# Kernel tuning notes

Measured on AMD Instinct MI355X. Metric: run time of the kernel, lower is better.

## Reference

```python
import jax, jax.numpy as jnp
import numpy as np

NB, S, D, B, T, KMAX = 7, 16, 128, 32, 2048, 31
KS = [31, 21, 15, 11, 7, 5, 3]  # per-band conv kernel sizes


def _ln(x, g, b, eps=1e-5):
    m = x.mean(-1, keepdims=True)
    v = ((x - m) ** 2).mean(-1, keepdims=True)
    return (x - m) * jax.lax.rsqrt(v + eps) * g + b


def setup_inputs() -> dict:
    key = jax.random.key(0)
    ks = jax.random.split(key, 18)
    n = lambda k, shape, s=0.02: jax.random.normal(k, shape, jnp.float32) * s
    # conv kernels zero-padded to KMAX=31; symmetric padding keeps SAME-conv
    # equivalent to Conv1d(kernel=k, padding=k//2)
    mask = np.zeros((NB, KMAX, 1, 1), np.float32)
    for i, k in enumerate(KS):
        off = (KMAX - k) // 2
        mask[i, off:off + k] = 1.0
    inp = {
        'x': jax.random.normal(ks[0], (B, T, S), jnp.float32),
        'conv_w': n(ks[1], (NB, KMAX, S, D)) * jnp.asarray(mask),
        'conv_b': n(ks[2], (NB, D)),
        'dec_g': jnp.ones((NB, D), jnp.float32),
        'dec_b': jnp.zeros((NB, D), jnp.float32),
        'n2_g': jnp.ones((NB, D), jnp.float32),
        'n2_b': jnp.zeros((NB, D), jnp.float32),
        'ffn_w1': n(ks[3], (NB, D, 2 * D)),
        'ffn_b1': n(ks[4], (NB, 2 * D)),
        'ffn_w2': n(ks[5], (NB, 2 * D, D)),
        'ffn_b2': n(ks[6], (NB, D)),
        'proj_w': n(ks[7], (NB, D, 4 * S)),
        'proj_b': n(ks[8], (NB, 4 * S)),
        'mix_w1': n(ks[9], (NB * 4 * S, 8 * S)),
        'mix_b1': n(ks[10], (8 * S,)),
        'mix_w2': n(ks[11], (8 * S, S)),
        'mix_b2': n(ks[12], (S,)),
    }
    return inp


def reference(x, conv_w, conv_b, dec_g, dec_b, n2_g, n2_b,
              ffn_w1, ffn_b1, ffn_w2, ffn_b2,
              proj_w, proj_b, mix_w1, mix_b1, mix_w2, mix_b2):
    # Spectral decomposition: per-band 1D conv + LayerNorm. [nb, B, T, D]
    conv1 = lambda w: jax.lax.conv_general_dilated(
        x, w, (1,), 'SAME', dimension_numbers=('NWC', 'WIO', 'NWC'))
    h = jax.vmap(conv1)(conv_w) + conv_b[:, None, None, :]
    h = _ln(h, dec_g[:, None, None, :], dec_b[:, None, None, :])
    # Band processors (empty history => residual FFN branch)
    z = _ln(h, n2_g[:, None, None, :], n2_b[:, None, None, :])
    u = jax.nn.gelu(jnp.einsum('nbtd,nde->nbte', z, ffn_w1)
                    + ffn_b1[:, None, None, :], approximate=False)
    band_out = h + (jnp.einsum('nbte,ned->nbtd', u, ffn_w2)
                    + ffn_b2[:, None, None, :])
    # Reconstruction: per-band projection, concat, mix MLP
    p = jnp.einsum('nbtd,ndp->nbtp', band_out, proj_w) + proj_b[:, None, None, :]
    cat = jnp.transpose(p, (1, 2, 0, 3)).reshape(x.shape[0], x.shape[1], -1)
    m = jax.nn.gelu(cat @ mix_w1 + mix_b1, approximate=False)
    return m @ mix_w2 + mix_b2
```

## Files before the change

kernel.cpp:

```cpp
#include <hip/hip_runtime.h>
#include <stdint.h>

#define NB   7
#define SIN  16
#define DD   128
#define BB   32
#define TT   2048
#define TM   64
#define KMAX 31

#define XWS  40
#define HS   136
#define US   264
#define PS   72

#define O_CWT 0
#define O_W1T 458752
#define O_W2T 688128
#define O_PT  917504
#define O_M1T 974848
#define O_M2T 1032192
#define W_TOTAL 1034240

typedef short v8s __attribute__((ext_vector_type(8)));
typedef float v4f __attribute__((ext_vector_type(4)));

__device__ __forceinline__ unsigned short f2b(float f) {
    unsigned u = __float_as_uint(f);
    u += 0x7fffu + ((u >> 16) & 1u);
    return (unsigned short)(u >> 16);
}
__device__ __forceinline__ float b2f(unsigned short h) {
    return __uint_as_float(((unsigned)h) << 16);
}
__device__ __forceinline__ float gelu_fast(float x) {
    return x / (1.f + __expf(-1.702f * x));
}
__device__ __forceinline__ float gelu_exact(float x) {
    return 0.5f * x * (1.f + erff(x * 0.70710678118654752f));
}

__global__ void prep_weights(const float* __restrict__ conv_w,
                             const float* __restrict__ ffn_w1,
                             const float* __restrict__ ffn_w2,
                             const float* __restrict__ proj_w,
                             const float* __restrict__ mix_w1,
                             const float* __restrict__ mix_w2,
                             unsigned short* __restrict__ wsb) {
    for (int i = blockIdx.x * 256 + threadIdx.x; i < W_TOTAL; i += gridDim.x * 256) {
        float v;
        int o = i;
        if (o < O_W1T) {
            int n = o / (128 * 512); int r = o % (128 * 512);
            int d = r / 512; int kf = r % 512;
            int k = kf >> 4, s = kf & 15;
            v = (k < KMAX) ? conv_w[((n * KMAX + k) * SIN + s) * DD + d] : 0.f;
        } else if ((o -= O_W1T) < (O_W2T - O_W1T)) {
            int n = o / (256 * 128); int r = o % (256 * 128);
            int e = r / 128; int k = r % 128;
            v = ffn_w1[(n * 128 + k) * 256 + e];
        } else if ((o -= (O_W2T - O_W1T)) < (O_PT - O_W2T)) {
            int n = o / (128 * 256); int r = o % (128 * 256);
            int d = r / 256; int e = r % 256;
            v = ffn_w2[(n * 256 + e) * 128 + d];
        } else if ((o -= (O_PT - O_W2T)) < (O_M1T - O_PT)) {
            int n = o / (64 * 128); int r = o % (64 * 128);
            int j = r / 128; int k = r % 128;
            v = proj_w[(n * 128 + k) * 64 + j];
        } else if ((o -= (O_M1T - O_PT)) < (O_M2T - O_M1T)) {
            int c = o / 448; int kk = o % 448;
            v = mix_w1[kk * 128 + c];
        } else {
            o -= (O_M2T - O_M1T);
            int o16 = o / 128; int c = o % 128;
            v = mix_w2[c * 16 + o16];
        }
        wsb[i] = f2b(v);
    }
}

__global__ __launch_bounds__(256, 2)
void fused_main(const float* __restrict__ x,
                const float* __restrict__ conv_b,
                const float* __restrict__ dec_g, const float* __restrict__ dec_b,
                const float* __restrict__ n2_g,  const float* __restrict__ n2_b,
                const float* __restrict__ ffn_b1, const float* __restrict__ ffn_b2,
                const float* __restrict__ proj_b,
                const float* __restrict__ mix_b1, const float* __restrict__ mix_b2,
                const unsigned short* __restrict__ wsb,
                float* __restrict__ out) {
    __shared__ __align__(16) unsigned short xw[95 * XWS];
    __shared__ __align__(16) unsigned short hbuf[TM * HS];
    __shared__ __align__(16) unsigned short zbuf[TM * HS];
    __shared__ __align__(16) unsigned short ubuf[TM * US];

    const int tid  = threadIdx.x;
    const int lane = tid & 63;
    const int w    = tid >> 6;
    const int l16  = lane & 15;
    const int quad = lane >> 4;
    const int bb   = blockIdx.x >> 5;
    const int t0   = (blockIdx.x & 31) * TM;

    const unsigned short* cwT = wsb + O_CWT;
    const unsigned short* w1T = wsb + O_W1T;
    const unsigned short* w2T = wsb + O_W2T;
    const unsigned short* pT  = wsb + O_PT;
    const unsigned short* m1T = wsb + O_M1T;
    const unsigned short* m2T = wsb + O_M2T;

    for (int i = tid; i < 95 * SIN; i += 256) {
        int r = i >> 4, s = i & 15;
        int t = t0 + r - 15;
        float v = (t >= 0 && t < TT) ? x[((long)bb * TT + t) * SIN + s] : 0.f;
        xw[r * XWS + s] = f2b(v);
    }

    v4f macc[4][2];
    #pragma unroll
    for (int a = 0; a < 4; a++)
        #pragma unroll
        for (int c = 0; c < 2; c++)
            macc[a][c] = (v4f){0.f, 0.f, 0.f, 0.f};

    __syncthreads();

    static const int lo_tab[NB] = {0, 64, 128, 160, 192, 192, 224};
    static const int hi_tab[NB] = {512, 416, 384, 352, 320, 288, 288};

    for (int n = 0; n < NB; ++n) {
        {
            v4f acc[4][2];
            #pragma unroll
            for (int mt = 0; mt < 4; mt++)
                #pragma unroll
                for (int nt = 0; nt < 2; nt++) acc[mt][nt] = (v4f){0.f, 0.f, 0.f, 0.f};
            const int colb = w * 32;
            const int lo = lo_tab[n], hi = hi_tab[n];
            for (int kf = lo; kf < hi; kf += 32) {
                const int tap  = (kf >> 4) + (quad >> 1);
                const int scol = (quad & 1) * 8;
                v8s a[4], bf[2];
                #pragma unroll
                for (int mt = 0; mt < 4; mt++)
                    a[mt] = *reinterpret_cast<const v8s*>(&xw[(mt * 16 + l16 + tap) * XWS + scol]);
                #pragma unroll
                for (int nt = 0; nt < 2; nt++)
                    bf[nt] = *reinterpret_cast<const v8s*>(
                        &cwT[(size_t)(n * 128 + colb + nt * 16 + l16) * 512 + kf + quad * 8]);
                #pragma unroll
                for (int mt = 0; mt < 4; mt++)
                    #pragma unroll
                    for (int nt = 0; nt < 2; nt++)
                        acc[mt][nt] = __builtin_amdgcn_mfma_f32_16x16x32_bf16(a[mt], bf[nt], acc[mt][nt], 0, 0, 0);
            }
            #pragma unroll
            for (int nt = 0; nt < 2; nt++) {
                const int col = colb + nt * 16 + l16;
                const float bias = conv_b[n * 128 + col];
                #pragma unroll
                for (int mt = 0; mt < 4; mt++)
                    #pragma unroll
                    for (int r = 0; r < 4; r++)
                        hbuf[(mt * 16 + quad * 4 + r) * HS + col] = f2b(acc[mt][nt][r] + bias);
            }
        }
        __syncthreads();

        {
            const int row = tid >> 2, q = tid & 3;
            float v[32], s1 = 0.f, s2 = 0.f;
            #pragma unroll
            for (int c8 = 0; c8 < 4; c8++) {
                v8s t8 = *reinterpret_cast<const v8s*>(&hbuf[row * HS + q * 32 + c8 * 8]);
                #pragma unroll
                for (int j = 0; j < 8; j++) {
                    float f = b2f((unsigned short)t8[j]);
                    v[c8 * 8 + j] = f; s1 += f; s2 += f * f;
                }
            }
            s1 += __shfl_xor(s1, 1); s2 += __shfl_xor(s2, 1);
            s1 += __shfl_xor(s1, 2); s2 += __shfl_xor(s2, 2);
            const float m1 = s1 * (1.f / 128.f);
            const float rs = rsqrtf(s2 * (1.f / 128.f) - m1 * m1 + 1e-5f);
            const float4* dg4 = (const float4*)(dec_g + n * 128);
            const float4* db4 = (const float4*)(dec_b + n * 128);
            float hv[32], t1 = 0.f, t2 = 0.f;
            #pragma unroll
            for (int c4 = 0; c4 < 8; c4++) {
                float4 g4 = dg4[q * 8 + c4], b4 = db4[q * 8 + c4];
                float ga[4] = {g4.x, g4.y, g4.z, g4.w};
                float ba[4] = {b4.x, b4.y, b4.z, b4.w};
                #pragma unroll
                for (int j = 0; j < 4; j++) {
                    float h = (v[c4 * 4 + j] - m1) * rs * ga[j] + ba[j];
                    hv[c4 * 4 + j] = h; t1 += h; t2 += h * h;
                    hbuf[row * HS + q * 32 + c4 * 4 + j] = f2b(h);
                }
            }
            t1 += __shfl_xor(t1, 1); t2 += __shfl_xor(t2, 1);
            t1 += __shfl_xor(t1, 2); t2 += __shfl_xor(t2, 2);
            const float m2 = t1 * (1.f / 128.f);
            const float rs2 = rsqrtf(t2 * (1.f / 128.f) - m2 * m2 + 1e-5f);
            const float4* ng4 = (const float4*)(n2_g + n * 128);
            const float4* nb4 = (const float4*)(n2_b + n * 128);
            #pragma unroll
            for (int c4 = 0; c4 < 8; c4++) {
                float4 g4 = ng4[q * 8 + c4], b4 = nb4[q * 8 + c4];
                float ga[4] = {g4.x, g4.y, g4.z, g4.w};
                float ba[4] = {b4.x, b4.y, b4.z, b4.w};
                #pragma unroll
                for (int j = 0; j < 4; j++) {
                    float z = (hv[c4 * 4 + j] - m2) * rs2 * ga[j] + ba[j];
                    zbuf[row * HS + q * 32 + c4 * 4 + j] = f2b(z);
                }
            }
        }
        __syncthreads();

        {
            v4f acc[4][4];
            #pragma unroll
            for (int mt = 0; mt < 4; mt++)
                #pragma unroll
                for (int et = 0; et < 4; et++) acc[mt][et] = (v4f){0.f, 0.f, 0.f, 0.f};
            const int eb = w * 64;
            #pragma unroll
            for (int kb = 0; kb < 128; kb += 32) {
                v8s a[4], bf[4];
                #pragma unroll
                for (int mt = 0; mt < 4; mt++)
                    a[mt] = *reinterpret_cast<const v8s*>(&zbuf[(mt * 16 + l16) * HS + kb + quad * 8]);
                #pragma unroll
                for (int et = 0; et < 4; et++)
                    bf[et] = *reinterpret_cast<const v8s*>(
                        &w1T[(size_t)(n * 256 + eb + et * 16 + l16) * 128 + kb + quad * 8]);
                #pragma unroll
                for (int mt = 0; mt < 4; mt++)
                    #pragma unroll
                    for (int et = 0; et < 4; et++)
                        acc[mt][et] = __builtin_amdgcn_mfma_f32_16x16x32_bf16(a[mt], bf[et], acc[mt][et], 0, 0, 0);
            }
            #pragma unroll
            for (int et = 0; et < 4; et++) {
                const int e = eb + et * 16 + l16;
                const float bias = ffn_b1[n * 256 + e];
                #pragma unroll
                for (int mt = 0; mt < 4; mt++)
                    #pragma unroll
                    for (int r = 0; r < 4; r++)
                        ubuf[(mt * 16 + quad * 4 + r) * US + e] = f2b(gelu_fast(acc[mt][et][r] + bias));
            }
        }
        __syncthreads();

        {
            v4f acc[4][2];
            #pragma unroll
            for (int mt = 0; mt < 4; mt++)
                #pragma unroll
                for (int nt = 0; nt < 2; nt++) acc[mt][nt] = (v4f){0.f, 0.f, 0.f, 0.f};
            const int dbs = w * 32;
            #pragma unroll
            for (int kb = 0; kb < 256; kb += 32) {
                v8s a[4], bf[2];
                #pragma unroll
                for (int mt = 0; mt < 4; mt++)
                    a[mt] = *reinterpret_cast<const v8s*>(&ubuf[(mt * 16 + l16) * US + kb + quad * 8]);
                #pragma unroll
                for (int nt = 0; nt < 2; nt++)
                    bf[nt] = *reinterpret_cast<const v8s*>(
                        &w2T[(size_t)(n * 128 + dbs + nt * 16 + l16) * 256 + kb + quad * 8]);
                #pragma unroll
                for (int mt = 0; mt < 4; mt++)
                    #pragma unroll
                    for (int nt = 0; nt < 2; nt++)
                        acc[mt][nt] = __builtin_amdgcn_mfma_f32_16x16x32_bf16(a[mt], bf[nt], acc[mt][nt], 0, 0, 0);
            }
            #pragma unroll
            for (int nt = 0; nt < 2; nt++) {
                const int col = dbs + nt * 16 + l16;
                const float bias = ffn_b2[n * 128 + col];
                #pragma unroll
                for (int mt = 0; mt < 4; mt++)
                    #pragma unroll
                    for (int r = 0; r < 4; r++) {
                        const int row = mt * 16 + quad * 4 + r;
                        float bo = acc[mt][nt][r] + bias + b2f(hbuf[row * HS + col]);
                        zbuf[row * HS + col] = f2b(bo);
                    }
            }
        }
        __syncthreads();

        {
            v4f acc[4];
            #pragma unroll
            for (int mt = 0; mt < 4; mt++) acc[mt] = (v4f){0.f, 0.f, 0.f, 0.f};
            const int j = w * 16 + l16;
            #pragma unroll
            for (int kb = 0; kb < 128; kb += 32) {
                v8s bf = *reinterpret_cast<const v8s*>(&pT[(size_t)(n * 64 + j) * 128 + kb + quad * 8]);
                #pragma unroll
                for (int mt = 0; mt < 4; mt++) {
                    v8s a = *reinterpret_cast<const v8s*>(&zbuf[(mt * 16 + l16) * HS + kb + quad * 8]);
                    acc[mt] = __builtin_amdgcn_mfma_f32_16x16x32_bf16(a, bf, acc[mt], 0, 0, 0);
                }
            }
            const float bias = proj_b[n * 64 + j];
            unsigned short* pb = ubuf;
            #pragma unroll
            for (int mt = 0; mt < 4; mt++)
                #pragma unroll
                for (int r = 0; r < 4; r++)
                    pb[(mt * 16 + quad * 4 + r) * PS + j] = f2b(acc[mt][r] + bias);
        }
        __syncthreads();

        {
            const unsigned short* pb = ubuf;
            #pragma unroll
            for (int kb = 0; kb < 64; kb += 32) {
                v8s a[4], bf[2];
                #pragma unroll
                for (int mt = 0; mt < 4; mt++)
                    a[mt] = *reinterpret_cast<const v8s*>(&pb[(mt * 16 + l16) * PS + kb + quad * 8]);
                #pragma unroll
                for (int nt = 0; nt < 2; nt++)
                    bf[nt] = *reinterpret_cast<const v8s*>(
                        &m1T[(size_t)(w * 32 + nt * 16 + l16) * 448 + n * 64 + kb + quad * 8]);
                #pragma unroll
                for (int mt = 0; mt < 4; mt++)
                    #pragma unroll
                    for (int nt = 0; nt < 2; nt++)
                        macc[mt][nt] = __builtin_amdgcn_mfma_f32_16x16x32_bf16(a[mt], bf[nt], macc[mt][nt], 0, 0, 0);
            }
        }
    }

    #pragma unroll
    for (int nt = 0; nt < 2; nt++) {
        const int col = w * 32 + nt * 16 + l16;
        const float bias = mix_b1[col];
        #pragma unroll
        for (int mt = 0; mt < 4; mt++)
            #pragma unroll
            for (int r = 0; r < 4; r++)
                zbuf[(mt * 16 + quad * 4 + r) * HS + col] = f2b(gelu_exact(macc[mt][nt][r] + bias));
    }
    __syncthreads();

    {
        v4f acc = (v4f){0.f, 0.f, 0.f, 0.f};
        #pragma unroll
        for (int kb = 0; kb < 128; kb += 32) {
            v8s a  = *reinterpret_cast<const v8s*>(&zbuf[(w * 16 + l16) * HS + kb + quad * 8]);
            v8s bf = *reinterpret_cast<const v8s*>(&m2T[(size_t)l16 * 128 + kb + quad * 8]);
            acc = __builtin_amdgcn_mfma_f32_16x16x32_bf16(a, bf, acc, 0, 0, 0);
        }
        const float bias = mix_b2[l16];
        #pragma unroll
        for (int r = 0; r < 4; r++) {
            const int row = w * 16 + quad * 4 + r;
            out[((long)bb * TT + t0 + row) * SIN + l16] = acc[r] + bias;
        }
    }
}

extern "C" void kernel_launch(void* const* d_in, const int* in_sizes, int n_in,
                              void* d_out, int out_size, void* d_ws, size_t ws_size,
                              hipStream_t stream) {
    (void)in_sizes; (void)n_in; (void)out_size; (void)ws_size;
    const float* x      = (const float*)d_in[0];
    const float* conv_w = (const float*)d_in[1];
    const float* conv_b = (const float*)d_in[2];
    const float* dec_g  = (const float*)d_in[3];
    const float* dec_b  = (const float*)d_in[4];
    const float* n2_g   = (const float*)d_in[5];
    const float* n2_b   = (const float*)d_in[6];
    const float* ffn_w1 = (const float*)d_in[7];
    const float* ffn_b1 = (const float*)d_in[8];
    const float* ffn_w2 = (const float*)d_in[9];
    const float* ffn_b2 = (const float*)d_in[10];
    const float* proj_w = (const float*)d_in[11];
    const float* proj_b = (const float*)d_in[12];
    const float* mix_w1 = (const float*)d_in[13];
    const float* mix_b1 = (const float*)d_in[14];
    const float* mix_w2 = (const float*)d_in[15];
    const float* mix_b2 = (const float*)d_in[16];
    unsigned short* wsb = (unsigned short*)d_ws;
    float* out = (float*)d_out;

    hipLaunchKernelGGL(prep_weights, dim3(512), dim3(256), 0, stream,
                       conv_w, ffn_w1, ffn_w2, proj_w, mix_w1, mix_w2, wsb);
    hipLaunchKernelGGL(fused_main, dim3(BB * (TT / TM)), dim3(256), 0, stream,
                       x, conv_b, dec_g, dec_b, n2_g, n2_b, ffn_b1, ffn_b2,
                       proj_b, mix_b1, mix_b2, wsb, out);
}
```

Measured before the change: 417.0 us.

## Give each wave its own 16-row tile and drop block-wide barriers

Each of the four waves now owns 16 rows of the 64-row tile across all 128/256 columns, instead of splitting the tile by column. LayerNorms are computed in registers with cross-lane shuffles, the h residual is kept packed in registers, and the FFN hidden dimension is processed in two halves through per-wave LDS scratch. This removes nearly all __syncthreads and shrinks LDS so occupancy can rise to 3 blocks per CU. The cost is that each wave reloads every weight B-fragment from global/L2 for its own rows, roughly quadrupling weight traffic per block, and register pressure goes up.

```diff
diff --git a/kernel.cpp b/kernel.cpp
--- a/kernel.cpp
+++ b/kernel.cpp
@@ -9,9 +9,9 @@
 #define TM   64
 #define KMAX 31
 
-#define XWS  40
-#define HS   136
-#define US   264
+#define XWS  24
+#define ZS   136
+#define US   136
 #define PS   72
 
 #define O_CWT 0
@@ -79,7 +79,7 @@
     }
 }
 
-__global__ __launch_bounds__(256, 2)
+__global__ __launch_bounds__(256, 3)
 void fused_main(const float* __restrict__ x,
                 const float* __restrict__ conv_b,
                 const float* __restrict__ dec_g, const float* __restrict__ dec_b,
@@ -90,9 +90,8 @@
                 const unsigned short* __restrict__ wsb,
                 float* __restrict__ out) {
     __shared__ __align__(16) unsigned short xw[95 * XWS];
-    __shared__ __align__(16) unsigned short hbuf[TM * HS];
-    __shared__ __align__(16) unsigned short zbuf[TM * HS];
-    __shared__ __align__(16) unsigned short ubuf[TM * US];
+    __shared__ __align__(16) unsigned short zbs[4][16 * ZS];
+    __shared__ __align__(16) unsigned short ubs[4][16 * US];
 
     const int tid  = threadIdx.x;
     const int lane = tid & 63;
@@ -102,6 +101,9 @@
     const int bb   = blockIdx.x >> 5;
     const int t0   = (blockIdx.x & 31) * TM;
 
+    unsigned short* zb = zbs[w];
+    unsigned short* ub = ubs[w];
+
     const unsigned short* cwT = wsb + O_CWT;
     const unsigned short* w1T = wsb + O_W1T;
     const unsigned short* w2T = wsb + O_W2T;
@@ -116,253 +118,215 @@
         xw[r * XWS + s] = f2b(v);
     }
 
-    v4f macc[4][2];
+    v4f macc[8];
     #pragma unroll
-    for (int a = 0; a < 4; a++)
-        #pragma unroll
-        for (int c = 0; c < 2; c++)
-            macc[a][c] = (v4f){0.f, 0.f, 0.f, 0.f};
+    for (int nt = 0; nt < 8; nt++) macc[nt] = (v4f){0.f, 0.f, 0.f, 0.f};
 
     __syncthreads();
 
     static const int lo_tab[NB] = {0, 64, 128, 160, 192, 192, 224};
     static const int hi_tab[NB] = {512, 416, 384, 352, 320, 288, 288};
 
+    const int arow = w * 16 + l16;
+
     for (int n = 0; n < NB; ++n) {
+        unsigned hpk[16];
+
         {
-            v4f acc[4][2];
-            #pragma unroll
-            for (int mt = 0; mt < 4; mt++)
-                #pragma unroll
-                for (int nt = 0; nt < 2; nt++) acc[mt][nt] = (v4f){0.f, 0.f, 0.f, 0.f};
-            const int colb = w * 32;
+            v4f hacc[8];
+            #pragma unroll
+            for (int nt = 0; nt < 8; nt++) hacc[nt] = (v4f){0.f, 0.f, 0.f, 0.f};
+            const unsigned short* cwn = cwT + (size_t)n * 128 * 512;
             const int lo = lo_tab[n], hi = hi_tab[n];
+            const int scol = (quad & 1) * 8;
             for (int kf = lo; kf < hi; kf += 32) {
-                const int tap  = (kf >> 4) + (quad >> 1);
-                const int scol = (quad & 1) * 8;
-                v8s a[4], bf[2];
-                #pragma unroll
-                for (int mt = 0; mt < 4; mt++)
-                    a[mt] = *reinterpret_cast<const v8s*>(&xw[(mt * 16 + l16 + tap) * XWS + scol]);
-                #pragma unroll
-                for (int nt = 0; nt < 2; nt++)
-                    bf[nt] = *reinterpret_cast<const v8s*>(
-                        &cwT[(size_t)(n * 128 + colb + nt * 16 + l16) * 512 + kf + quad * 8]);
-                #pragma unroll
-                for (int mt = 0; mt < 4; mt++)
-                    #pragma unroll
-                    for (int nt = 0; nt < 2; nt++)
-                        acc[mt][nt] = __builtin_amdgcn_mfma_f32_16x16x32_bf16(a[mt], bf[nt], acc[mt][nt], 0, 0, 0);
-            }
-            #pragma unroll
-            for (int nt = 0; nt < 2; nt++) {
-                const int col = colb + nt * 16 + l16;
-                const float bias = conv_b[n * 128 + col];
-                #pragma unroll
-                for (int mt = 0; mt < 4; mt++)
-                    #pragma unroll
-                    for (int r = 0; r < 4; r++)
-                        hbuf[(mt * 16 + quad * 4 + r) * HS + col] = f2b(acc[mt][nt][r] + bias);
-            }
-        }
-        __syncthreads();
+                const int tap = (kf >> 4) + (quad >> 1);
+                v8s a = *reinterpret_cast<const v8s*>(&xw[(arow + tap) * XWS + scol]);
+                #pragma unroll
+                for (int nt = 0; nt < 8; nt++) {
+                    v8s bf = *reinterpret_cast<const v8s*>(
+                        &cwn[(size_t)(nt * 16 + l16) * 512 + kf + quad * 8]);
+                    hacc[nt] = __builtin_amdgcn_mfma_f32_16x16x32_bf16(a, bf, hacc[nt], 0, 0, 0);
+                }
+            }
+            float cb[8], dg[8], db[8], ng[8], nb[8];
+            #pragma unroll
+            for (int nt = 0; nt < 8; nt++) {
+                const int c = n * 128 + nt * 16 + l16;
+                cb[nt] = conv_b[c]; dg[nt] = dec_g[c]; db[nt] = dec_b[c];
+                ng[nt] = n2_g[c];   nb[nt] = n2_b[c];
+            }
+            float s1[4] = {0.f,0.f,0.f,0.f}, s2[4] = {0.f,0.f,0.f,0.f};
+            #pragma unroll
+            for (int nt = 0; nt < 8; nt++)
+                #pragma unroll
+                for (int r = 0; r < 4; r++) {
+                    float v = hacc[nt][r] + cb[nt];
+                    hacc[nt][r] = v; s1[r] += v; s2[r] += v * v;
+                }
+            #pragma unroll
+            for (int m = 1; m <= 8; m <<= 1)
+                #pragma unroll
+                for (int r = 0; r < 4; r++) {
+                    s1[r] += __shfl_xor(s1[r], m);
+                    s2[r] += __shfl_xor(s2[r], m);
+                }
+            float mu[4], rs[4];
+            #pragma unroll
+            for (int r = 0; r < 4; r++) {
+                mu[r] = s1[r] * (1.f / 128.f);
+                rs[r] = rsqrtf(s2[r] * (1.f / 128.f) - mu[r] * mu[r] + 1e-5f);
+            }
+            float t1[4] = {0.f,0.f,0.f,0.f}, t2[4] = {0.f,0.f,0.f,0.f};
+            #pragma unroll
+            for (int nt = 0; nt < 8; nt++)
+                #pragma unroll
+                for (int r = 0; r < 4; r++) {
+                    float h = (hacc[nt][r] - mu[r]) * rs[r] * dg[nt] + db[nt];
+                    hacc[nt][r] = h; t1[r] += h; t2[r] += h * h;
+                }
+            #pragma unroll
+            for (int m = 1; m <= 8; m <<= 1)
+                #pragma unroll
+                for (int r = 0; r < 4; r++) {
+                    t1[r] += __shfl_xor(t1[r], m);
+                    t2[r] += __shfl_xor(t2[r], m);
+                }
+            float mu2[4], rs2[4];
+            #pragma unroll
+            for (int r = 0; r < 4; r++) {
+                mu2[r] = t1[r] * (1.f / 128.f);
+                rs2[r] = rsqrtf(t2[r] * (1.f / 128.f) - mu2[r] * mu2[r] + 1e-5f);
+            }
+            #pragma unroll
+            for (int nt = 0; nt < 8; nt++) {
+                #pragma unroll
+                for (int rr = 0; rr < 2; rr++) {
+                    float h0 = hacc[nt][2 * rr],     h1 = hacc[nt][2 * rr + 1];
+                    hpk[nt * 2 + rr] = (unsigned)f2b(h0) | ((unsigned)f2b(h1) << 16);
+                }
+                #pragma unroll
+                for (int r = 0; r < 4; r++) {
+                    float z = (hacc[nt][r] - mu2[r]) * rs2[r] * ng[nt] + nb[nt];
+                    zb[(quad * 4 + r) * ZS + nt * 16 + l16] = f2b(z);
+                }
+            }
+        }
+
+        v4f acc2[8];
+        #pragma unroll
+        for (int dt = 0; dt < 8; dt++) acc2[dt] = (v4f){0.f, 0.f, 0.f, 0.f};
+        #pragma unroll
+        for (int eh = 0; eh < 2; ++eh) {
+            v4f ua[8];
+            #pragma unroll
+            for (int nt = 0; nt < 8; nt++) ua[nt] = (v4f){0.f, 0.f, 0.f, 0.f};
+            const unsigned short* w1n = w1T + ((size_t)n * 256 + eh * 128) * 128;
+            #pragma unroll
+            for (int kb = 0; kb < 128; kb += 32) {
+                v8s a = *reinterpret_cast<const v8s*>(&zb[l16 * ZS + kb + quad * 8]);
+                #pragma unroll
+                for (int nt = 0; nt < 8; nt++) {
+                    v8s bf = *reinterpret_cast<const v8s*>(
+                        &w1n[(size_t)(nt * 16 + l16) * 128 + kb + quad * 8]);
+                    ua[nt] = __builtin_amdgcn_mfma_f32_16x16x32_bf16(a, bf, ua[nt], 0, 0, 0);
+                }
+            }
+            #pragma unroll
+            for (int nt = 0; nt < 8; nt++) {
+                const float b1 = ffn_b1[n * 256 + eh * 128 + nt * 16 + l16];
+                #pragma unroll
+                for (int r = 0; r < 4; r++)
+                    ub[(quad * 4 + r) * US + nt * 16 + l16] = f2b(gelu_fast(ua[nt][r] + b1));
+            }
+            const unsigned short* w2n = w2T + (size_t)n * 128 * 256 + eh * 128;
+            #pragma unroll
+            for (int kb = 0; kb < 128; kb += 32) {
+                v8s a = *reinterpret_cast<const v8s*>(&ub[l16 * US + kb + quad * 8]);
+                #pragma unroll
+                for (int dt = 0; dt < 8; dt++) {
+                    v8s bf = *reinterpret_cast<const v8s*>(
+                        &w2n[(size_t)(dt * 16 + l16) * 256 + kb + quad * 8]);
+                    acc2[dt] = __builtin_amdgcn_mfma_f32_16x16x32_bf16(a, bf, acc2[dt], 0, 0, 0);
+                }
+            }
+        }
+
+        #pragma unroll
+        for (int dt = 0; dt < 8; dt++) {
+            const float b2v = ffn_b2[n * 128 + dt * 16 + l16];
+            #pragma unroll
+            for (int rr = 0; rr < 2; rr++) {
+                unsigned hp = hpk[dt * 2 + rr];
+                float h0 = __uint_as_float(hp << 16);
+                float h1 = __uint_as_float(hp & 0xffff0000u);
+                float bo0 = acc2[dt][2 * rr]     + b2v + h0;
+                float bo1 = acc2[dt][2 * rr + 1] + b2v + h1;
+                zb[(quad * 4 + 2 * rr)     * ZS + dt * 16 + l16] = f2b(bo0);
+                zb[(quad * 4 + 2 * rr + 1) * ZS + dt * 16 + l16] = f2b(bo1);
+            }
+        }
 
         {
-            const int row = tid >> 2, q = tid & 3;
-            float v[32], s1 = 0.f, s2 = 0.f;
-            #pragma unroll
-            for (int c8 = 0; c8 < 4; c8++) {
-                v8s t8 = *reinterpret_cast<const v8s*>(&hbuf[row * HS + q * 32 + c8 * 8]);
-                #pragma unroll
-                for (int j = 0; j < 8; j++) {
-                    float f = b2f((unsigned short)t8[j]);
-                    v[c8 * 8 + j] = f; s1 += f; s2 += f * f;
-                }
-            }
-            s1 += __shfl_xor(s1, 1); s2 += __shfl_xor(s2, 1);
-            s1 += __shfl_xor(s1, 2); s2 += __shfl_xor(s2, 2);
-            const float m1 = s1 * (1.f / 128.f);
-            const float rs = rsqrtf(s2 * (1.f / 128.f) - m1 * m1 + 1e-5f);
-            const float4* dg4 = (const float4*)(dec_g + n * 128);
-            const float4* db4 = (const float4*)(dec_b + n * 128);
-            float hv[32], t1 = 0.f, t2 = 0.f;
-            #pragma unroll
-            for (int c4 = 0; c4 < 8; c4++) {
-                float4 g4 = dg4[q * 8 + c4], b4 = db4[q * 8 + c4];
-                float ga[4] = {g4.x, g4.y, g4.z, g4.w};
-                float ba[4] = {b4.x, b4.y, b4.z, b4.w};
-                #pragma unroll
-                for (int j = 0; j < 4; j++) {
-                    float h = (v[c4 * 4 + j] - m1) * rs * ga[j] + ba[j];
-                    hv[c4 * 4 + j] = h; t1 += h; t2 += h * h;
-                    hbuf[row * HS + q * 32 + c4 * 4 + j] = f2b(h);
-                }
-            }
-            t1 += __shfl_xor(t1, 1); t2 += __shfl_xor(t2, 1);
-            t1 += __shfl_xor(t1, 2); t2 += __shfl_xor(t2, 2);
-            const float m2 = t1 * (1.f / 128.f);
-            const float rs2 = rsqrtf(t2 * (1.f / 128.f) - m2 * m2 + 1e-5f);
-            const float4* ng4 = (const float4*)(n2_g + n * 128);
-            const float4* nb4 = (const float4*)(n2_b + n * 128);
-            #pragma unroll
-            for (int c4 = 0; c4 < 8; c4++) {
-                float4 g4 = ng4[q * 8 + c4], b4 = nb4[q * 8 + c4];
-                float ga[4] = {g4.x, g4.y, g4.z, g4.w};
-                float ba[4] = {b4.x, b4.y, b4.z, b4.w};
-                #pragma unroll
-                for (int j = 0; j < 4; j++) {
-                    float z = (hv[c4 * 4 + j] - m2) * rs2 * ga[j] + ba[j];
-                    zbuf[row * HS + q * 32 + c4 * 4 + j] = f2b(z);
-                }
-            }
-        }
-        __syncthreads();
+            v4f pa[4];
+            #pragma unroll
+            for (int jt = 0; jt < 4; jt++) pa[jt] = (v4f){0.f, 0.f, 0.f, 0.f};
+            const unsigned short* pn = pT + (size_t)n * 64 * 128;
+            #pragma unroll
+            for (int kb = 0; kb < 128; kb += 32) {
+                v8s a = *reinterpret_cast<const v8s*>(&zb[l16 * ZS + kb + quad * 8]);
+                #pragma unroll
+                for (int jt = 0; jt < 4; jt++) {
+                    v8s bf = *reinterpret_cast<const v8s*>(
+                        &pn[(size_t)(jt * 16 + l16) * 128 + kb + quad * 8]);
+                    pa[jt] = __builtin_amdgcn_mfma_f32_16x16x32_bf16(a, bf, pa[jt], 0, 0, 0);
+                }
+            }
+            #pragma unroll
+            for (int jt = 0; jt < 4; jt++) {
+                const float pbv = proj_b[n * 64 + jt * 16 + l16];
+                #pragma unroll
+                for (int r = 0; r < 4; r++)
+                    ub[(quad * 4 + r) * PS + jt * 16 + l16] = f2b(pa[jt][r] + pbv);
+            }
+        }
 
         {
-            v4f acc[4][4];
-            #pragma unroll
-            for (int mt = 0; mt < 4; mt++)
-                #pragma unroll
-                for (int et = 0; et < 4; et++) acc[mt][et] = (v4f){0.f, 0.f, 0.f, 0.f};
-            const int eb = w * 64;
-            #pragma unroll
-            for (int kb = 0; kb < 128; kb += 32) {
-                v8s a[4], bf[4];
-                #pragma unroll
-                for (int mt = 0; mt < 4; mt++)
-                    a[mt] = *reinterpret_cast<const v8s*>(&zbuf[(mt * 16 + l16) * HS + kb + quad * 8]);
-                #pragma unroll
-                for (int et = 0; et < 4; et++)
-                    bf[et] = *reinterpret_cast<const v8s*>(
-                        &w1T[(size_t)(n * 256 + eb + et * 16 + l16) * 128 + kb + quad * 8]);
-                #pragma unroll
-                for (int mt = 0; mt < 4; mt++)
-                    #pragma unroll
-                    for (int et = 0; et < 4; et++)
-                        acc[mt][et] = __builtin_amdgcn_mfma_f32_16x16x32_bf16(a[mt], bf[et], acc[mt][et], 0, 0, 0);
-            }
-            #pragma unroll
-            for (int et = 0; et < 4; et++) {
-                const int e = eb + et * 16 + l16;
-                const float bias = ffn_b1[n * 256 + e];
-                #pragma unroll
-                for (int mt = 0; mt < 4; mt++)
-                    #pragma unroll
-                    for (int r = 0; r < 4; r++)
-                        ubuf[(mt * 16 + quad * 4 + r) * US + e] = f2b(gelu_fast(acc[mt][et][r] + bias));
-            }
-        }
-        __syncthreads();
-
-        {
-            v4f acc[4][2];
-            #pragma unroll
-            for (int mt = 0; mt < 4; mt++)
-                #pragma unroll
-                for (int nt = 0; nt < 2; nt++) acc[mt][nt] = (v4f){0.f, 0.f, 0.f, 0.f};
-            const int dbs = w * 32;
-            #pragma unroll
-            for (int kb = 0; kb < 256; kb += 32) {
-                v8s a[4], bf[2];
-                #pragma unroll
-                for (int mt = 0; mt < 4; mt++)
-                    a[mt] = *reinterpret_cast<const v8s*>(&ubuf[(mt * 16 + l16) * US + kb + quad * 8]);
-                #pragma unroll
-                for (int nt = 0; nt < 2; nt++)
-                    bf[nt] = *reinterpret_cast<const v8s*>(
-                        &w2T[(size_t)(n * 128 + dbs + nt * 16 + l16) * 256 + kb + quad * 8]);
-                #pragma unroll
-                for (int mt = 0; mt < 4; mt++)
-                    #pragma unroll
-                    for (int nt = 0; nt < 2; nt++)
-                        acc[mt][nt] = __builtin_amdgcn_mfma_f32_16x16x32_bf16(a[mt], bf[nt], acc[mt][nt], 0, 0, 0);
-            }
-            #pragma unroll
-            for (int nt = 0; nt < 2; nt++) {
-                const int col = dbs + nt * 16 + l16;
-                const float bias = ffn_b2[n * 128 + col];
-                #pragma unroll
-                for (int mt = 0; mt < 4; mt++)
-                    #pragma unroll
-                    for (int r = 0; r < 4; r++) {
-                        const int row = mt * 16 + quad * 4 + r;
-                        float bo = acc[mt][nt][r] + bias + b2f(hbuf[row * HS + col]);
-                        zbuf[row * HS + col] = f2b(bo);
-                    }
-            }
-        }
-        __syncthreads();
-
-        {
-            v4f acc[4];
-            #pragma unroll
-            for (int mt = 0; mt < 4; mt++) acc[mt] = (v4f){0.f, 0.f, 0.f, 0.f};
-            const int j = w * 16 + l16;
-            #pragma unroll
-            for (int kb = 0; kb < 128; kb += 32) {
-                v8s bf = *reinterpret_cast<const v8s*>(&pT[(size_t)(n * 64 + j) * 128 + kb + quad * 8]);
-                #pragma unroll
-                for (int mt = 0; mt < 4; mt++) {
-                    v8s a = *reinterpret_cast<const v8s*>(&zbuf[(mt * 16 + l16) * HS + kb + quad * 8]);
-                    acc[mt] = __builtin_amdgcn_mfma_f32_16x16x32_bf16(a, bf, acc[mt], 0, 0, 0);
-                }
-            }
-            const float bias = proj_b[n * 64 + j];
-            unsigned short* pb = ubuf;
-            #pragma unroll
-            for (int mt = 0; mt < 4; mt++)
-                #pragma unroll
-                for (int r = 0; r < 4; r++)
-                    pb[(mt * 16 + quad * 4 + r) * PS + j] = f2b(acc[mt][r] + bias);
-        }
-        __syncthreads();
-
-        {
-            const unsigned short* pb = ubuf;
+            const unsigned short* m1n = m1T + n * 64;
             #pragma unroll
             for (int kb = 0; kb < 64; kb += 32) {
-                v8s a[4], bf[2];
-                #pragma unroll
-                for (int mt = 0; mt < 4; mt++)
-                    a[mt] = *reinterpret_cast<const v8s*>(&pb[(mt * 16 + l16) * PS + kb + quad * 8]);
-                #pragma unroll
-                for (int nt = 0; nt < 2; nt++)
-                    bf[nt] = *reinterpret_cast<const v8s*>(
-                        &m1T[(size_t)(w * 32 + nt * 16 + l16) * 448 + n * 64 + kb + quad * 8]);
-                #pragma unroll
-                for (int mt = 0; mt < 4; mt++)
-                    #pragma unroll
-                    for (int nt = 0; nt < 2; nt++)
-                        macc[mt][nt] = __builtin_amdgcn_mfma_f32_16x16x32_bf16(a[mt], bf[nt], macc[mt][nt], 0, 0, 0);
+                v8s a = *reinterpret_cast<const v8s*>(&ub[l16 * PS + kb + quad * 8]);
+                #pragma unroll
+                for (int nt = 0; nt < 8; nt++) {
+                    v8s bf = *reinterpret_cast<const v8s*>(
+                        &m1n[(size_t)(nt * 16 + l16) * 448 + kb + quad * 8]);
+                    macc[nt] = __builtin_amdgcn_mfma_f32_16x16x32_bf16(a, bf, macc[nt], 0, 0, 0);
+                }
             }
         }
     }
 
     #pragma unroll
-    for (int nt = 0; nt < 2; nt++) {
-        const int col = w * 32 + nt * 16 + l16;
-        const float bias = mix_b1[col];
-        #pragma unroll
-        for (int mt = 0; mt < 4; mt++)
-            #pragma unroll
-            for (int r = 0; r < 4; r++)
-                zbuf[(mt * 16 + quad * 4 + r) * HS + col] = f2b(gelu_exact(macc[mt][nt][r] + bias));
-    }
-    __syncthreads();
+    for (int nt = 0; nt < 8; nt++) {
+        const float mb1 = mix_b1[nt * 16 + l16];
+        #pragma unroll
+        for (int r = 0; r < 4; r++)
+            ub[(quad * 4 + r) * US + nt * 16 + l16] = f2b(gelu_exact(macc[nt][r] + mb1));
+    }
 
     {
-        v4f acc = (v4f){0.f, 0.f, 0.f, 0.f};
+        v4f oacc = (v4f){0.f, 0.f, 0.f, 0.f};
         #pragma unroll
         for (int kb = 0; kb < 128; kb += 32) {
-            v8s a  = *reinterpret_cast<const v8s*>(&zbuf[(w * 16 + l16) * HS + kb + quad * 8]);
+            v8s a  = *reinterpret_cast<const v8s*>(&ub[l16 * US + kb + quad * 8]);
             v8s bf = *reinterpret_cast<const v8s*>(&m2T[(size_t)l16 * 128 + kb + quad * 8]);
-            acc = __builtin_amdgcn_mfma_f32_16x16x32_bf16(a, bf, acc, 0, 0, 0);
-        }
-        const float bias = mix_b2[l16];
+            oacc = __builtin_amdgcn_mfma_f32_16x16x32_bf16(a, bf, oacc, 0, 0, 0);
+        }
+        const float ob = mix_b2[l16];
         #pragma unroll
         for (int r = 0; r < 4; r++) {
             const int row = w * 16 + quad * 4 + r;
-            out[((long)bb * TT + t0 + row) * SIN + l16] = acc[r] + bias;
+            out[((long)bb * TT + t0 + row) * SIN + l16] = oacc[r] + ob;
         }
     }
 }
@@ -391,7 +355,7 @@
     unsigned short* wsb = (unsigned short*)d_ws;
     float* out = (float*)d_out;
 
-    hipLaunchKernelGGL(prep_weights, dim3(512), dim3(256), 0, stream,
+    hipLaunchKernelGGL(prep_weights, dim3(1024), dim3(256), 0, stream,
                        conv_w, ffn_w1, ffn_w2, proj_w, mix_w1, mix_w2, wsb);
     hipLaunchKernelGGL(fused_main, dim3(BB * (TT / TM)), dim3(256), 0, stream,
                        x, conv_b, dec_g, dec_b, n2_g, n2_b, ffn_b1, ffn_b2,
```

Result: slower. 1.265 ms (+203.4%).
